# Kernel tuning notes

Hardware: AMD Instinct MI355X
Metric: run time of the kernel (lower is better)

## Reference

```python
import jax, jax.numpy as jnp
import numpy as np

V, B, C, NS, H, W = 3, 2, 64, 32, 128, 128


def setup_inputs() -> dict:
    key = jax.random.key(0)
    k1, k2 = jax.random.split(key, 2)
    features = jax.random.normal(k1, (V, B, C, H, W), dtype=jnp.float32)
    f = 1.1 * W
    K = np.array([[f, 0.0, (W - 1) / 2.0],
                  [0.0, f, (H - 1) / 2.0],
                  [0.0, 0.0, 1.0]], dtype=np.float32)
    intrinsics = jnp.asarray(np.broadcast_to(K, (V, B, 3, 3)).copy())
    c2w = np.tile(np.eye(4, dtype=np.float32), (V, B, 1, 1))
    rng = np.random.default_rng(0)
    for v in range(1, V):
        for b in range(B):
            th = rng.uniform(-0.03, 0.03)
            Ry = np.array([[np.cos(th), 0.0, np.sin(th)],
                           [0.0, 1.0, 0.0],
                           [-np.sin(th), 0.0, np.cos(th)]], dtype=np.float32)
            c2w[v, b, :3, :3] = Ry
            c2w[v, b, :3, 3] = rng.uniform(-0.1, 0.1, size=3).astype(np.float32)
    cam_to_world = jnp.asarray(c2w)
    scale_hypo = jnp.broadcast_to(jnp.linspace(0.5, 1.5, NS, dtype=jnp.float32), (B, NS)) + jnp.zeros((B, NS), jnp.float32)
    depth_init = 2.0 + 4.0 * jax.random.uniform(k2, (B, H, W), dtype=jnp.float32)
    return {"features": features, "intrinsics": intrinsics, "cam_to_world": cam_to_world,
            "scale_hypo": scale_hypo, "depth_init": depth_init}


def _grid_sample_zeros(feat, grid):
    """torch F.grid_sample(mode='bilinear', padding_mode='zeros', align_corners=False)."""
    Bn, Cn, Hn, Wn = feat.shape
    ix = ((grid[..., 0] + 1.0) * Wn - 1.0) * 0.5
    iy = ((grid[..., 1] + 1.0) * Hn - 1.0) * 0.5
    x0 = jnp.floor(ix); y0 = jnp.floor(iy)
    x1 = x0 + 1.0; y1 = y0 + 1.0
    wx1 = ix - x0; wx0 = 1.0 - wx1
    wy1 = iy - y0; wy0 = 1.0 - wy1
    featf = feat.reshape(Bn, Cn, Hn * Wn)

    def corner(xc, yc, w):
        valid = (xc >= 0) & (xc <= Wn - 1) & (yc >= 0) & (yc <= Hn - 1)
        xi = jnp.clip(xc, 0, Wn - 1).astype(jnp.int32)
        yi = jnp.clip(yc, 0, Hn - 1).astype(jnp.int32)
        idx = (yi * Wn + xi).reshape(Bn, 1, -1)
        v = jnp.take_along_axis(featf, idx, axis=2)  # (B,C,Npts)
        return v * (w * valid).reshape(Bn, 1, -1)

    out = (corner(x0, y0, wx0 * wy0) + corner(x1, y0, wx1 * wy0)
           + corner(x0, y1, wx0 * wy1) + corner(x1, y1, wx1 * wy1))
    return out.reshape(Bn, Cn, grid.shape[1], grid.shape[2])


def _homo_warp(src_feat, scale_hypo, depth_init, src_K, src_c2w, ref_K, ref_c2w):
    # src_feat (B,C,H,W); depth_init (B,1,H,W); returns (B,C,Ns,H,W)
    Bn, Cn, Hn, Wn = src_feat.shape
    Ns = scale_hypo.shape[1]

    def build_grid():
        src_w2c = jnp.linalg.inv(src_c2w)
        ref_w2c = jnp.linalg.inv(ref_c2w)
        # original clones world_to_cam and only replaces the top-left 3x3 with K,
        # so the w2c translation column is kept inside the 'intrinsics' matrix
        src_P = src_w2c.at[:, :3, :3].set(src_K)
        ref_P = ref_w2c.at[:, :3, :3].set(ref_K)
        proj = (src_P @ src_w2c) @ jnp.linalg.inv(ref_P @ ref_w2c)
        rot = proj[:, :3, :3]
        trans = proj[:, :3, 3]
        depth = depth_init.reshape(Bn, 1, 1, Hn * Wn) * scale_hypo[:, None, :, None]  # (B,1,Ns,HW)
        # NOTE: original builds both grid axes from arange(height); valid since H==W
        y, x = jnp.meshgrid(jnp.arange(Hn, dtype=jnp.float32),
                            jnp.arange(Wn, dtype=jnp.float32), indexing='ij')
        xyz = jnp.stack([x.ravel(), y.ravel(), jnp.ones(Hn * Wn, dtype=jnp.float32)])  # (3,HW)
        rot_xyz = jnp.einsum('bij,jn->bin', rot, xyz)                         # (B,3,HW)
        proj_xyz = rot_xyz[:, :, None, :] * depth + trans[:, :, None, None]   # (B,3,Ns,HW)
        proj_xy = proj_xyz[:, :2] / proj_xyz[:, 2:3]
        gx = proj_xy[:, 0] / ((Wn - 1) / 2.0) - 1.0
        gy = proj_xy[:, 1] / ((Hn - 1) / 2.0) - 1.0
        return jnp.stack([gx, gy], axis=-1).reshape(Bn, Ns * Hn, Wn, 2)

    grid = jax.lax.stop_gradient(build_grid())  # torch computes the grid under no_grad
    warped = _grid_sample_zeros(src_feat, grid)
    return warped.reshape(Bn, Cn, Ns, Hn, Wn)


def reference(features, intrinsics, cam_to_world, scale_hypo, depth_init):
    num_views = features.shape[0]
    Bn, Cn, Hn, Wn = features.shape[1:]
    Ns = scale_hypo.shape[1]
    ref_K, ref_c2w = intrinsics[0], cam_to_world[0]
    # faithfully replicate torch's in-place ref_volume.sub_() bug:
    # ref accumulates the subtraction of every previously-warped volume
    ref_running = jnp.broadcast_to(features[0][:, :, None], (Bn, Cn, Ns, Hn, Wn))
    cost = jnp.zeros((Bn, Ns, Hn, Wn), dtype=features.dtype)
    for v in range(1, num_views):
        warped = _homo_warp(features[v], scale_hypo, depth_init[:, None],
                            intrinsics[v], cam_to_world[v], ref_K, ref_c2w)
        ref_running = ref_running - warped
        cost = cost + jnp.sqrt(jnp.sum(ref_running * ref_running, axis=1))  # L2 over C
    cost = cost / (num_views - 1)
    cost = jnp.mean(cost, axis=(2, 3))          # (B, Nscale)
    prob = jax.nn.softmax(cost, axis=1)
    return jnp.sum(prob * scale_hypo, axis=1)   # (B,)
```

## Files before the change

kernel.cpp:

```cpp
#include <hip/hip_runtime.h>
#include <math.h>

constexpr int NV = 3;
constexpr int NB = 2;
constexpr int NC = 64;
constexpr int NSC = 32;
constexpr int NH = 128;
constexpr int NW = 128;
constexpr int NSB = 16;

typedef _Float16 h2_t __attribute__((ext_vector_type(2)));

template <int CTRL>
__device__ __forceinline__ float dpp_add(float x) {
    int s = __builtin_amdgcn_update_dpp(0, __float_as_int(x), CTRL, 0xf, 0xf, true);
    return x + __int_as_float(s);
}

__device__ __forceinline__ float dot2acc(h2_t a, float acc) {
#if __has_builtin(__builtin_amdgcn_fdot2)
    return __builtin_amdgcn_fdot2(a, a, acc, false);
#else
    float x = (float)a.x, y = (float)a.y;
    return acc + x * x + y * y;
#endif
}

__device__ void inv4x4(const double* m, double* out) {
    double inv[16];
    inv[0]  =  m[5]*m[10]*m[15] - m[5]*m[11]*m[14] - m[9]*m[6]*m[15] + m[9]*m[7]*m[14] + m[13]*m[6]*m[11] - m[13]*m[7]*m[10];
    inv[4]  = -m[4]*m[10]*m[15] + m[4]*m[11]*m[14] + m[8]*m[6]*m[15] - m[8]*m[7]*m[14] - m[12]*m[6]*m[11] + m[12]*m[7]*m[10];
    inv[8]  =  m[4]*m[9]*m[15]  - m[4]*m[11]*m[13] - m[8]*m[5]*m[15] + m[8]*m[7]*m[13] + m[12]*m[5]*m[11] - m[12]*m[7]*m[9];
    inv[12] = -m[4]*m[9]*m[14]  + m[4]*m[10]*m[13] + m[8]*m[5]*m[14] - m[8]*m[6]*m[13] - m[12]*m[5]*m[10] + m[12]*m[6]*m[9];
    inv[1]  = -m[1]*m[10]*m[15] + m[1]*m[11]*m[14] + m[9]*m[2]*m[15] - m[9]*m[3]*m[14] - m[13]*m[2]*m[11] + m[13]*m[3]*m[10];
    inv[5]  =  m[0]*m[10]*m[15] - m[0]*m[11]*m[14] - m[8]*m[2]*m[15] + m[8]*m[3]*m[14] + m[12]*m[2]*m[11] - m[12]*m[3]*m[10];
    inv[9]  = -m[0]*m[9]*m[15]  + m[0]*m[11]*m[13] + m[8]*m[1]*m[15] - m[8]*m[3]*m[13] - m[12]*m[1]*m[11] + m[12]*m[3]*m[9];
    inv[13] =  m[0]*m[9]*m[14]  - m[0]*m[10]*m[13] - m[8]*m[1]*m[14] + m[8]*m[2]*m[13] + m[12]*m[1]*m[10] - m[12]*m[2]*m[9];
    inv[2]  =  m[1]*m[6]*m[15]  - m[1]*m[7]*m[14]  - m[5]*m[2]*m[15] + m[5]*m[3]*m[14] + m[13]*m[2]*m[7]  - m[13]*m[3]*m[6];
    inv[6]  = -m[0]*m[6]*m[15]  + m[0]*m[7]*m[14]  + m[4]*m[2]*m[15] - m[4]*m[3]*m[14] - m[12]*m[2]*m[7]  + m[12]*m[3]*m[6];
    inv[10] =  m[0]*m[5]*m[15]  - m[0]*m[7]*m[13]  - m[4]*m[1]*m[15] + m[4]*m[3]*m[13] + m[12]*m[1]*m[7]  - m[12]*m[3]*m[5];
    inv[14] = -m[0]*m[5]*m[14]  + m[0]*m[6]*m[13]  + m[4]*m[1]*m[14] - m[4]*m[2]*m[13] - m[12]*m[1]*m[6]  + m[12]*m[2]*m[5];
    inv[3]  = -m[1]*m[6]*m[11]  + m[1]*m[7]*m[10]  + m[5]*m[2]*m[11] - m[5]*m[3]*m[10] - m[9]*m[2]*m[7]   + m[9]*m[3]*m[6];
    inv[7]  =  m[0]*m[6]*m[11]  - m[0]*m[7]*m[10]  - m[4]*m[2]*m[11] + m[4]*m[3]*m[10] + m[8]*m[2]*m[7]   - m[8]*m[3]*m[6];
    inv[11] = -m[0]*m[5]*m[11]  + m[0]*m[7]*m[9]   + m[4]*m[1]*m[11] - m[4]*m[3]*m[9]  - m[8]*m[1]*m[7]   + m[8]*m[3]*m[5];
    inv[15] =  m[0]*m[5]*m[10]  - m[0]*m[6]*m[9]   - m[4]*m[1]*m[10] + m[4]*m[2]*m[9]  + m[8]*m[1]*m[6]   - m[8]*m[2]*m[5];
    double det = m[0]*inv[0] + m[1]*inv[4] + m[2]*inv[8] + m[3]*inv[12];
    det = 1.0 / det;
    for (int i = 0; i < 16; ++i) out[i] = inv[i] * det;
}

__device__ void mat4mul(const double* a, const double* b, double* o) {
    for (int i = 0; i < 4; ++i)
        for (int j = 0; j < 4; ++j) {
            double s = 0.0;
            for (int k = 0; k < 4; ++k) s += a[i*4+k] * b[k*4+j];
            o[i*4+j] = s;
        }
}

__global__ __launch_bounds__(256) void transpose_kernel(const float* __restrict__ in,
                                                        unsigned int* __restrict__ out,
                                                        const float* __restrict__ intr,
                                                        const float* __restrict__ c2w,
                                                        float* __restrict__ rt,
                                                        float* __restrict__ cost,
                                                        unsigned int* __restrict__ counter) {
    __shared__ float tile[NC][NW + 1];
    const int y  = blockIdx.x;
    const int vb = blockIdx.y;

    for (int i = threadIdx.x; i < NC * NW; i += 256) {
        int c = i >> 7;
        int x = i & (NW - 1);
        tile[c][x] = in[((size_t)(vb * NC + c) * NH + y) * NW + x];
    }
    __syncthreads();
    unsigned int* dst = out + ((size_t)vb * NH + y) * NW * (NC / 2);
    for (int i = threadIdx.x; i < NW * (NC / 2); i += 256) {
        int x  = i >> 5;
        int cp = i & 31;
        h2_t h = { (_Float16)tile[2 * cp][x], (_Float16)tile[2 * cp + 1][x] };
        dst[x * (NC / 2) + cp] = __builtin_bit_cast(unsigned int, h);
    }

    if (blockIdx.x == 0 && blockIdx.y == 0) {
        int t = threadIdx.x;
        if (t >= 4 && t < 4 + NB * NSC) cost[t - 4] = 0.f;
        if (t == 4 + NB * NSC) *counter = 0u;
        if (t < 2 * NB) {
            int vi = t >> 1;
            int b  = t & 1;
            int v  = vi + 1;

            double src_c2w[16], ref_c2w[16];
            for (int i = 0; i < 16; ++i) {
                src_c2w[i] = (double)c2w[(v * NB + b) * 16 + i];
                ref_c2w[i] = (double)c2w[(0 * NB + b) * 16 + i];
            }
            double src_w2c[16], ref_w2c[16];
            inv4x4(src_c2w, src_w2c);
            inv4x4(ref_c2w, ref_w2c);

            double srcP[16], refP[16];
            for (int i = 0; i < 16; ++i) { srcP[i] = src_w2c[i]; refP[i] = ref_w2c[i]; }
            for (int r = 0; r < 3; ++r)
                for (int c = 0; c < 3; ++c) {
                    srcP[r*4+c] = (double)intr[(v * NB + b) * 9 + r*3 + c];
                    refP[r*4+c] = (double)intr[(0 * NB + b) * 9 + r*3 + c];
                }

            double M1[16], M2[16], M2inv[16];
            mat4mul(srcP, src_w2c, M1);
            mat4mul(refP, ref_w2c, M2);
            inv4x4(M2, M2inv);
            double proj[16];
            mat4mul(M1, M2inv, proj);

            float* o = rt + (vi * NB + b) * 12;
            o[0] = (float)proj[0];  o[1] = (float)proj[1];  o[2]  = (float)proj[2];
            o[3] = (float)proj[4];  o[4] = (float)proj[5];  o[5]  = (float)proj[6];
            o[6] = (float)proj[8];  o[7] = (float)proj[9];  o[8]  = (float)proj[10];
            o[9] = (float)proj[3];  o[10] = (float)proj[7]; o[11] = (float)proj[11];
        }
    }
}

__global__ __launch_bounds__(256) void cost_kernel(
    const unsigned int* __restrict__ ftb,
    const float* __restrict__ depth,
    const float* __restrict__ scale,
    const float* __restrict__ rt,
    float* __restrict__ cost,
    unsigned int* __restrict__ counter,
    float* __restrict__ outp,
    int total_blocks)
{
    const int tid  = threadIdx.x;
    const int lane = tid & 63;
    const int wv   = tid >> 6;
    const int grp  = lane >> 3;
    const int gl   = lane & 7;
    const int nsg  = blockIdx.y;
    const int b    = blockIdx.z;

    const int p = blockIdx.x * 32 + wv * 8 + grp;
    const int x = p & (NW - 1);
    const int y = p >> 7;
    const float fx = (float)x;
    const float fy = (float)y;

    const float d0 = depth[(b * NH + y) * NW + x];

    const uint4* f0q = (const uint4*)(ftb) + ((size_t)(0 * NB + b) * NH * NW + p) * 8 + gl;
    const uint4* v1q = (const uint4*)(ftb) + ((size_t)(1 * NB + b) * NH * NW) * 8 + gl;
    const uint4* v2q = (const uint4*)(ftb) + ((size_t)(2 * NB + b) * NH * NW) * 8 + gl;

    const uint4 f0u = *f0q;
    const h2_t* f0h = (const h2_t*)&f0u;

    float R0[12], R1[12];
#pragma unroll
    for (int k = 0; k < 12; ++k) {
        R0[k] = rt[(0 * NB + b) * 12 + k];
        R1[k] = rt[(1 * NB + b) * 12 + k];
    }
    const float ax0 = R0[0] * fx + R0[1] * fy + R0[2];
    const float ay0 = R0[3] * fx + R0[4] * fy + R0[5];
    const float az0 = R0[6] * fx + R0[7] * fy + R0[8];
    const float ax1 = R1[0] * fx + R1[1] * fy + R1[2];
    const float ay1 = R1[3] * fx + R1[4] * fy + R1[5];
    const float az1 = R1[6] * fx + R1[7] * fy + R1[8];

    const float CXY = 64.0f / 63.5f;

    __shared__ float red[4][NSB];

#pragma unroll 4
    for (int nsub = 0; nsub < NSB; ++nsub) {
        const float s = scale[b * NSC + nsg * NSB + nsub];
        const float d = d0 * s;

        int   ti[2][4];
        float tw[2][4];
#pragma unroll
        for (int vi = 0; vi < 2; ++vi) {
            float px = (vi ? ax1 : ax0) * d + (vi ? R1[9]  : R0[9]);
            float py = (vi ? ay1 : ay0) * d + (vi ? R1[10] : R0[10]);
            float pz = (vi ? az1 : az0) * d + (vi ? R1[11] : R0[11]);
            float invz = __builtin_amdgcn_rcpf(pz);
            float ix = (px * invz) * CXY - 0.5f;
            float iy = (py * invz) * CXY - 0.5f;

            float x0f = floorf(ix), y0f = floorf(iy);
            float wx1 = ix - x0f, wx0 = 1.f - wx1;
            float wy1 = iy - y0f, wy0 = 1.f - wy1;

            float mx0 = (x0f >= 0.f  && x0f <= 127.f) ? wx0 : 0.f;
            float mx1 = (x0f >= -1.f && x0f <= 126.f) ? wx1 : 0.f;
            float my0 = (y0f >= 0.f  && y0f <= 127.f) ? wy0 : 0.f;
            float my1 = (y0f >= -1.f && y0f <= 126.f) ? wy1 : 0.f;

            int xi0 = (int)fminf(fmaxf(x0f, 0.f), 127.f);
            int yi0 = (int)fminf(fmaxf(y0f, 0.f), 127.f);
            int xo = (x0f >= 0.f && x0f <= 126.f) ? 8 : 0;
            int yo = (y0f >= 0.f && y0f <= 126.f) ? NW * 8 : 0;

            int base = (yi0 * NW + xi0) * 8;
            ti[vi][0] = base;
            ti[vi][1] = base + xo;
            ti[vi][2] = base + yo;
            ti[vi][3] = base + yo + xo;
            tw[vi][0] = mx0 * my0;
            tw[vi][1] = mx1 * my0;
            tw[vi][2] = mx0 * my1;
            tw[vi][3] = mx1 * my1;
        }

        uint4 t0 = v1q[ti[0][0]];
        uint4 t1 = v1q[ti[0][1]];
        uint4 t2 = v1q[ti[0][2]];
        uint4 t3 = v1q[ti[0][3]];
        uint4 u0 = v2q[ti[1][0]];
        uint4 u1 = v2q[ti[1][1]];
        uint4 u2 = v2q[ti[1][2]];
        uint4 u3 = v2q[ti[1][3]];

        _Float16 w00 = (_Float16)(-tw[0][0]), w01 = (_Float16)(-tw[0][1]);
        _Float16 w02 = (_Float16)(-tw[0][2]), w03 = (_Float16)(-tw[0][3]);
        _Float16 w10 = (_Float16)(-tw[1][0]), w11 = (_Float16)(-tw[1][1]);
        _Float16 w12 = (_Float16)(-tw[1][2]), w13 = (_Float16)(-tw[1][3]);
        h2_t h00 = {w00, w00}, h01 = {w01, w01}, h02 = {w02, w02}, h03 = {w03, w03};
        h2_t h10 = {w10, w10}, h11 = {w11, w11}, h12 = {w12, w12}, h13 = {w13, w13};

        const h2_t* p0 = (const h2_t*)&t0;
        const h2_t* p1 = (const h2_t*)&t1;
        const h2_t* p2 = (const h2_t*)&t2;
        const h2_t* p3 = (const h2_t*)&t3;
        const h2_t* q0 = (const h2_t*)&u0;
        const h2_t* q1 = (const h2_t*)&u1;
        const h2_t* q2 = (const h2_t*)&u2;
        const h2_t* q3 = (const h2_t*)&u3;

        h2_t r[4];
        float sq1 = 0.f, sq2 = 0.f;
#pragma unroll
        for (int j = 0; j < 4; ++j) {
            h2_t rr = f0h[j];
            rr += p0[j] * h00;
            rr += p1[j] * h01;
            rr += p2[j] * h02;
            rr += p3[j] * h03;
            r[j] = rr;
            sq1 = dot2acc(rr, sq1);
        }
#pragma unroll
        for (int j = 0; j < 4; ++j) {
            h2_t rr = r[j];
            rr += q0[j] * h10;
            rr += q1[j] * h11;
            rr += q2[j] * h12;
            rr += q3[j] * h13;
            sq2 = dot2acc(rr, sq2);
        }

        sq1 = dpp_add<0x111>(sq1);
        sq1 = dpp_add<0x112>(sq1);
        sq1 = dpp_add<0x114>(sq1);
        sq2 = dpp_add<0x111>(sq2);
        sq2 = dpp_add<0x112>(sq2);
        sq2 = dpp_add<0x114>(sq2);
        float sv = sqrtf(sq1) + sqrtf(sq2);
        sv = dpp_add<0x118>(sv);
        sv = dpp_add<0x142>(sv);
        sv = dpp_add<0x143>(sv);
        if (lane == 63) red[wv][nsub] = sv;
    }

    __syncthreads();
    if (tid < NSB) {
        float t = red[0][tid] + red[1][tid] + red[2][tid] + red[3][tid];
        atomicAdd(&cost[b * NSC + nsg * NSB + tid], t * (0.5f / (float)(NH * NW)));
        __threadfence();
    }
    __syncthreads();

    __shared__ unsigned int lastflag;
    if (tid == 0) {
        unsigned int prev = atomicAdd(counter, 1u);
        lastflag = (prev == (unsigned int)(total_blocks - 1)) ? 1u : 0u;
    }
    __syncthreads();
    if (lastflag && tid < NB * NSC) {
        __threadfence();
        int bb = tid >> 5;
        int ns = tid & 31;
        float c  = atomicAdd(&cost[bb * NSC + ns], 0.0f);
        float sv = scale[bb * NSC + ns];

        float m = c;
#pragma unroll
        for (int mk = 1; mk < 32; mk <<= 1) m = fmaxf(m, __shfl_xor(m, mk, 64));
        float e = __expf(c - m);
        float sum = e;
#pragma unroll
        for (int mk = 1; mk < 32; mk <<= 1) sum += __shfl_xor(sum, mk, 64);
        float val = (e / sum) * sv;
#pragma unroll
        for (int mk = 1; mk < 32; mk <<= 1) val += __shfl_xor(val, mk, 64);
        if (ns == 0) outp[bb] = val;
    }
}

extern "C" void kernel_launch(void* const* d_in, const int* in_sizes, int n_in,
                              void* d_out, int out_size, void* d_ws, size_t ws_size,
                              hipStream_t stream) {
    const float* features   = (const float*)d_in[0];
    const float* intrinsics = (const float*)d_in[1];
    const float* cam2world  = (const float*)d_in[2];
    const float* scale_hypo = (const float*)d_in[3];
    const float* depth_init = (const float*)d_in[4];
    float* out = (float*)d_out;

    unsigned int* ftb = (unsigned int*)d_ws;
    float* rt   = (float*)(ftb + (size_t)NV * NB * NH * NW * (NC / 2));
    float* cost = rt + 2 * NB * 12;
    unsigned int* counter = (unsigned int*)(cost + NB * NSC);

    dim3 tgrid(NH, NV * NB);
    transpose_kernel<<<tgrid, 256, 0, stream>>>(features, ftb, intrinsics, cam2world,
                                                rt, cost, counter);

    dim3 cgrid(NH * NW / 32, NSC / NSB, NB);
    int total_blocks = cgrid.x * cgrid.y * cgrid.z;
    cost_kernel<<<cgrid, 256, 0, stream>>>(ftb, depth_init, scale_hypo, rt,
                                           cost, counter, out, total_blocks);
}
```

Before: 156.6 us.

## Precompute warp geometry cooperatively in LDS and software-pipeline gather loads

The projection and bilinear-weight math, previously repeated by all 8 lanes of each pixel group, is now computed once per (pixel, scale, view) by all 256 threads. The results are stored as packed half-precision records in shared memory. The main loop then reads these records and issues the gather loads for the next scale hypothesis before computing the current one, double-buffering the register data to hide memory latency. A launch-bounds occupancy hint of 4 is added. The trade-offs are more LDS use, an extra barrier, and higher register pressure from the prefetched uint4 values.

```diff
diff --git a/kernel.cpp b/kernel.cpp
--- a/kernel.cpp
+++ b/kernel.cpp
@@ -23,6 +23,15 @@
 #else
     float x = (float)a.x, y = (float)a.y;
     return acc + x * x + y * y;
+#endif
+}
+
+__device__ __forceinline__ h2_t pack2(float a, float b) {
+#if __has_builtin(__builtin_amdgcn_cvt_pkrtz)
+    return __builtin_bit_cast(h2_t, __builtin_amdgcn_cvt_pkrtz(a, b));
+#else
+    h2_t r = { (_Float16)a, (_Float16)b };
+    return r;
 #endif
 }
 
@@ -125,7 +134,36 @@
     }
 }
 
-__global__ __launch_bounds__(256) void cost_kernel(
+struct alignas(16) GeomRec {
+    int base;
+    int xoyo;
+    unsigned int w01;
+    unsigned int w23;
+};
+
+struct G4 {
+    int t0, t1, t2, t3;
+    h2_t w0s, w1s, w2s, w3s;
+};
+
+__device__ __forceinline__ G4 expand(GeomRec g) {
+    G4 o;
+    int xo = g.xoyo & 0xffff;
+    int yo = g.xoyo >> 16;
+    o.t0 = g.base;
+    o.t1 = g.base + xo;
+    o.t2 = g.base + yo;
+    o.t3 = g.base + yo + xo;
+    h2_t w01 = __builtin_bit_cast(h2_t, g.w01);
+    h2_t w23 = __builtin_bit_cast(h2_t, g.w23);
+    o.w0s = h2_t{w01.x, w01.x};
+    o.w1s = h2_t{w01.y, w01.y};
+    o.w2s = h2_t{w23.x, w23.x};
+    o.w3s = h2_t{w23.y, w23.y};
+    return o;
+}
+
+__global__ __launch_bounds__(256, 4) void cost_kernel(
     const unsigned int* __restrict__ ftb,
     const float* __restrict__ depth,
     const float* __restrict__ scale,
@@ -138,128 +176,128 @@
     const int tid  = threadIdx.x;
     const int lane = tid & 63;
     const int wv   = tid >> 6;
-    const int grp  = lane >> 3;
-    const int gl   = lane & 7;
     const int nsg  = blockIdx.y;
     const int b    = blockIdx.z;
 
-    const int p = blockIdx.x * 32 + wv * 8 + grp;
-    const int x = p & (NW - 1);
-    const int y = p >> 7;
-    const float fx = (float)x;
-    const float fy = (float)y;
-
-    const float d0 = depth[(b * NH + y) * NW + x];
-
-    const uint4* f0q = (const uint4*)(ftb) + ((size_t)(0 * NB + b) * NH * NW + p) * 8 + gl;
+    __shared__ float s_lds[NSB];
+    __shared__ float d_lds[32];
+    __shared__ GeomRec geom[2][NSB][32];
+    __shared__ float red[4][NSB];
+
+    if (tid < NSB) s_lds[tid] = scale[b * NSC + nsg * NSB + tid];
+    if (tid < 32)  d_lds[tid] = depth[b * NH * NW + blockIdx.x * 32 + tid];
+    __syncthreads();
+
+    {
+        float R0[12], R1[12];
+#pragma unroll
+        for (int k = 0; k < 12; ++k) {
+            R0[k] = rt[(0 * NB + b) * 12 + k];
+            R1[k] = rt[(1 * NB + b) * 12 + k];
+        }
+        const float CXY = 64.0f / 63.5f;
+
+#pragma unroll
+        for (int pp = 0; pp < 2; ++pp) {
+            int pr   = tid + pp * 256;
+            int nsub = pr >> 5;
+            int pix  = pr & 31;
+            int gp   = blockIdx.x * 32 + pix;
+            float fx = (float)(gp & (NW - 1));
+            float fy = (float)(gp >> 7);
+            float d  = d_lds[pix] * s_lds[nsub];
+
+#pragma unroll
+            for (int vi = 0; vi < 2; ++vi) {
+                const float* R = vi ? R1 : R0;
+                float px = (R[0] * fx + R[1] * fy + R[2]) * d + R[9];
+                float py = (R[3] * fx + R[4] * fy + R[5]) * d + R[10];
+                float pz = (R[6] * fx + R[7] * fy + R[8]) * d + R[11];
+                float invz = __builtin_amdgcn_rcpf(pz);
+                float ix = (px * invz) * CXY - 0.5f;
+                float iy = (py * invz) * CXY - 0.5f;
+
+                float x0f = floorf(ix), y0f = floorf(iy);
+                float wx1 = ix - x0f, wx0 = 1.f - wx1;
+                float wy1 = iy - y0f, wy0 = 1.f - wy1;
+
+                float mx0 = (x0f >= 0.f  && x0f <= 127.f) ? wx0 : 0.f;
+                float mx1 = (x0f >= -1.f && x0f <= 126.f) ? wx1 : 0.f;
+                float my0 = (y0f >= 0.f  && y0f <= 127.f) ? wy0 : 0.f;
+                float my1 = (y0f >= -1.f && y0f <= 126.f) ? wy1 : 0.f;
+
+                int xi0 = (int)fminf(fmaxf(x0f, 0.f), 127.f);
+                int yi0 = (int)fminf(fmaxf(y0f, 0.f), 127.f);
+                int xo  = (x0f >= 0.f && x0f <= 126.f) ? 8 : 0;
+                int yo  = (y0f >= 0.f && y0f <= 126.f) ? NW * 8 : 0;
+
+                GeomRec g;
+                g.base = (yi0 * NW + xi0) * 8;
+                g.xoyo = xo | (yo << 16);
+                g.w01  = __builtin_bit_cast(unsigned int, pack2(-(mx0 * my0), -(mx1 * my0)));
+                g.w23  = __builtin_bit_cast(unsigned int, pack2(-(mx0 * my1), -(mx1 * my1)));
+                geom[vi][nsub][pix] = g;
+            }
+        }
+    }
+    __syncthreads();
+
+    const int grp = lane >> 3;
+    const int gl  = lane & 7;
+    const int pix2 = wv * 8 + grp;
+
+    const uint4* f0q = (const uint4*)(ftb) +
+        ((size_t)(0 * NB + b) * NH * NW + blockIdx.x * 32 + pix2) * 8 + gl;
     const uint4* v1q = (const uint4*)(ftb) + ((size_t)(1 * NB + b) * NH * NW) * 8 + gl;
     const uint4* v2q = (const uint4*)(ftb) + ((size_t)(2 * NB + b) * NH * NW) * 8 + gl;
 
     const uint4 f0u = *f0q;
     const h2_t* f0h = (const h2_t*)&f0u;
 
-    float R0[12], R1[12];
-#pragma unroll
-    for (int k = 0; k < 12; ++k) {
-        R0[k] = rt[(0 * NB + b) * 12 + k];
-        R1[k] = rt[(1 * NB + b) * 12 + k];
-    }
-    const float ax0 = R0[0] * fx + R0[1] * fy + R0[2];
-    const float ay0 = R0[3] * fx + R0[4] * fy + R0[5];
-    const float az0 = R0[6] * fx + R0[7] * fy + R0[8];
-    const float ax1 = R1[0] * fx + R1[1] * fy + R1[2];
-    const float ay1 = R1[3] * fx + R1[4] * fy + R1[5];
-    const float az1 = R1[6] * fx + R1[7] * fy + R1[8];
-
-    const float CXY = 64.0f / 63.5f;
-
-    __shared__ float red[4][NSB];
-
-#pragma unroll 4
+    G4 ea = expand(geom[0][0][pix2]);
+    G4 eb = expand(geom[1][0][pix2]);
+    uint4 a0 = v1q[ea.t0], a1 = v1q[ea.t1], a2 = v1q[ea.t2], a3 = v1q[ea.t3];
+    uint4 b0 = v2q[eb.t0], b1 = v2q[eb.t1], b2 = v2q[eb.t2], b3 = v2q[eb.t3];
+
+#pragma unroll
     for (int nsub = 0; nsub < NSB; ++nsub) {
-        const float s = scale[b * NSC + nsg * NSB + nsub];
-        const float d = d0 * s;
-
-        int   ti[2][4];
-        float tw[2][4];
-#pragma unroll
-        for (int vi = 0; vi < 2; ++vi) {
-            float px = (vi ? ax1 : ax0) * d + (vi ? R1[9]  : R0[9]);
-            float py = (vi ? ay1 : ay0) * d + (vi ? R1[10] : R0[10]);
-            float pz = (vi ? az1 : az0) * d + (vi ? R1[11] : R0[11]);
-            float invz = __builtin_amdgcn_rcpf(pz);
-            float ix = (px * invz) * CXY - 0.5f;
-            float iy = (py * invz) * CXY - 0.5f;
-
-            float x0f = floorf(ix), y0f = floorf(iy);
-            float wx1 = ix - x0f, wx0 = 1.f - wx1;
-            float wy1 = iy - y0f, wy0 = 1.f - wy1;
-
-            float mx0 = (x0f >= 0.f  && x0f <= 127.f) ? wx0 : 0.f;
-            float mx1 = (x0f >= -1.f && x0f <= 126.f) ? wx1 : 0.f;
-            float my0 = (y0f >= 0.f  && y0f <= 127.f) ? wy0 : 0.f;
-            float my1 = (y0f >= -1.f && y0f <= 126.f) ? wy1 : 0.f;
-
-            int xi0 = (int)fminf(fmaxf(x0f, 0.f), 127.f);
-            int yi0 = (int)fminf(fmaxf(y0f, 0.f), 127.f);
-            int xo = (x0f >= 0.f && x0f <= 126.f) ? 8 : 0;
-            int yo = (y0f >= 0.f && y0f <= 126.f) ? NW * 8 : 0;
-
-            int base = (yi0 * NW + xi0) * 8;
-            ti[vi][0] = base;
-            ti[vi][1] = base + xo;
-            ti[vi][2] = base + yo;
-            ti[vi][3] = base + yo + xo;
-            tw[vi][0] = mx0 * my0;
-            tw[vi][1] = mx1 * my0;
-            tw[vi][2] = mx0 * my1;
-            tw[vi][3] = mx1 * my1;
-        }
-
-        uint4 t0 = v1q[ti[0][0]];
-        uint4 t1 = v1q[ti[0][1]];
-        uint4 t2 = v1q[ti[0][2]];
-        uint4 t3 = v1q[ti[0][3]];
-        uint4 u0 = v2q[ti[1][0]];
-        uint4 u1 = v2q[ti[1][1]];
-        uint4 u2 = v2q[ti[1][2]];
-        uint4 u3 = v2q[ti[1][3]];
-
-        _Float16 w00 = (_Float16)(-tw[0][0]), w01 = (_Float16)(-tw[0][1]);
-        _Float16 w02 = (_Float16)(-tw[0][2]), w03 = (_Float16)(-tw[0][3]);
-        _Float16 w10 = (_Float16)(-tw[1][0]), w11 = (_Float16)(-tw[1][1]);
-        _Float16 w12 = (_Float16)(-tw[1][2]), w13 = (_Float16)(-tw[1][3]);
-        h2_t h00 = {w00, w00}, h01 = {w01, w01}, h02 = {w02, w02}, h03 = {w03, w03};
-        h2_t h10 = {w10, w10}, h11 = {w11, w11}, h12 = {w12, w12}, h13 = {w13, w13};
-
-        const h2_t* p0 = (const h2_t*)&t0;
-        const h2_t* p1 = (const h2_t*)&t1;
-        const h2_t* p2 = (const h2_t*)&t2;
-        const h2_t* p3 = (const h2_t*)&t3;
-        const h2_t* q0 = (const h2_t*)&u0;
-        const h2_t* q1 = (const h2_t*)&u1;
-        const h2_t* q2 = (const h2_t*)&u2;
-        const h2_t* q3 = (const h2_t*)&u3;
+        G4 na, nb;
+        uint4 c0, c1, c2, c3, e0, e1, e2, e3;
+        if (nsub + 1 < NSB) {
+            na = expand(geom[0][nsub + 1][pix2]);
+            nb = expand(geom[1][nsub + 1][pix2]);
+            c0 = v1q[na.t0]; c1 = v1q[na.t1]; c2 = v1q[na.t2]; c3 = v1q[na.t3];
+            e0 = v2q[nb.t0]; e1 = v2q[nb.t1]; e2 = v2q[nb.t2]; e3 = v2q[nb.t3];
+        }
+
+        const h2_t* pA0 = (const h2_t*)&a0;
+        const h2_t* pA1 = (const h2_t*)&a1;
+        const h2_t* pA2 = (const h2_t*)&a2;
+        const h2_t* pA3 = (const h2_t*)&a3;
+        const h2_t* pB0 = (const h2_t*)&b0;
+        const h2_t* pB1 = (const h2_t*)&b1;
+        const h2_t* pB2 = (const h2_t*)&b2;
+        const h2_t* pB3 = (const h2_t*)&b3;
 
         h2_t r[4];
         float sq1 = 0.f, sq2 = 0.f;
 #pragma unroll
         for (int j = 0; j < 4; ++j) {
             h2_t rr = f0h[j];
-            rr += p0[j] * h00;
-            rr += p1[j] * h01;
-            rr += p2[j] * h02;
-            rr += p3[j] * h03;
+            rr += pA0[j] * ea.w0s;
+            rr += pA1[j] * ea.w1s;
+            rr += pA2[j] * ea.w2s;
+            rr += pA3[j] * ea.w3s;
             r[j] = rr;
             sq1 = dot2acc(rr, sq1);
         }
 #pragma unroll
         for (int j = 0; j < 4; ++j) {
             h2_t rr = r[j];
-            rr += q0[j] * h10;
-            rr += q1[j] * h11;
-            rr += q2[j] * h12;
-            rr += q3[j] * h13;
+            rr += pB0[j] * eb.w0s;
+            rr += pB1[j] * eb.w1s;
+            rr += pB2[j] * eb.w2s;
+            rr += pB3[j] * eb.w3s;
             sq2 = dot2acc(rr, sq2);
         }
 
@@ -274,6 +312,10 @@
         sv = dpp_add<0x142>(sv);
         sv = dpp_add<0x143>(sv);
         if (lane == 63) red[wv][nsub] = sv;
+
+        ea = na; eb = nb;
+        a0 = c0; a1 = c1; a2 = c2; a3 = c3;
+        b0 = e0; b1 = e1; b2 = e2; b3 = e3;
     }
 
     __syncthreads();
```

Result: no change. 156.6 us (-0.1%).
